# Optimization experiments

Hardware: AMD Instinct MI355X
Metric: run time of the kernel (lower is better)

Reference implementation:

```python
import jax, jax.numpy as jnp
import numpy as np

DIM = 768
NUM_HEADS = 12
HEAD_DIM = DIM // NUM_HEADS
SCALE = HEAD_DIM ** -0.5


def setup_inputs() -> dict:
    key = jax.random.key(0)
    ks = jax.random.split(key, 9)
    B, L, C = 4, 1024, DIM
    x = jax.random.normal(ks[0], (B, L, C), jnp.float32)
    q_ape = jax.random.normal(ks[1], (1, L, C), jnp.float32)
    k_ape = jax.random.normal(ks[2], (1, L, C), jnp.float32)
    attn_pos = jax.random.normal(ks[3], (1, NUM_HEADS, L, L), jnp.float32)
    s = C ** -0.5
    # torch Linear weights: (out_features, in_features)
    Wq = jax.random.normal(ks[4], (C, C), jnp.float32) * s
    Wk = jax.random.normal(ks[5], (C, C), jnp.float32) * s
    Wv = jax.random.normal(ks[6], (C, C), jnp.float32) * s
    Wp = jax.random.normal(ks[7], (C, C), jnp.float32) * s
    bp = jax.random.normal(ks[8], (C,), jnp.float32) * 0.01
    return {"x": x, "q_ape": q_ape, "k_ape": k_ape, "attn_pos": attn_pos,
            "Wq": Wq, "Wk": Wk, "Wv": Wv, "Wp": Wp, "bp": bp}


def _split_heads(t):
    # (B, L, C) -> (B, H, L, D)
    B, L, C = t.shape
    return t.reshape(B, L, NUM_HEADS, HEAD_DIM).transpose(0, 2, 1, 3)


def reference(x, q_ape, k_ape, attn_pos, Wq, Wk, Wv, Wp, bp):
    B, L, C = x.shape
    q = _split_heads((x + q_ape) @ Wq.T)          # (B,H,L,D)
    k = _split_heads((x + k_ape) @ Wk.T)          # (B,H,L,D)
    v = _split_heads(x @ Wv.T)                    # (B,H,L,D)
    attn = jnp.einsum('bhqd,bhkd->bhqk', q, k) * SCALE + attn_pos
    attn = jax.nn.softmax(attn, axis=-1)
    out = jnp.einsum('bhqk,bhkd->bhqd', attn, v)  # (B,H,L,D)
    out = out.transpose(0, 2, 1, 3).reshape(B, L, C)
    return out @ Wp.T + bp
```

## Files before the change

### kernel.cpp

```cpp
#include <hip/hip_runtime.h>
#include <stdint.h>

#define NH 12
#define HD 64
#define NB 4
#define SEQ 1024
#define CDIM 768
#define MTOT (NB*SEQ)
#define MC   (MTOT*CDIM)
#define LC   (SEQ*CDIM)
#define WSZ  (CDIM*CDIM)
#define LST  104
#define EST  136
#define L2E  1.44269504f

typedef __attribute__((ext_vector_type(4))) float f32x4;
typedef __attribute__((ext_vector_type(8))) __bf16 bf16x8;
typedef __attribute__((ext_vector_type(8))) short short8;
typedef __attribute__((ext_vector_type(4))) unsigned short ushort4v;
typedef unsigned short u16;

static __device__ __forceinline__ f32x4 mfma16(short8 a, short8 b, f32x4 c) {
  return __builtin_amdgcn_mfma_f32_16x16x32_bf16(
      __builtin_bit_cast(bf16x8, a), __builtin_bit_cast(bf16x8, b), c, 0, 0, 0);
}
static __device__ __forceinline__ u16 f2bf(float f) {
  unsigned u = __float_as_uint(f);
  u += 0x7FFFu + ((u >> 16) & 1u);
  return (u16)(u >> 16);
}
static __device__ __forceinline__ float bf2f(u16 h) {
  return __uint_as_float(((unsigned)h) << 16);
}
static __device__ __forceinline__ void lds_load16(const void* g, void* l) {
  __builtin_amdgcn_global_load_lds(
      (const __attribute__((address_space(1))) void*)g,
      (__attribute__((address_space(3))) void*)l, 16, 0, 0);
}
static __device__ __forceinline__ void barrier_lgkm() {
  __builtin_amdgcn_s_waitcnt(0xC07F);
  __builtin_amdgcn_s_barrier();
}

#define PREP_BLKS (MC / 4 / 256)
#define CONV_N4   ((4 * WSZ + CDIM) / 4)
#define CONV_BLKS ((CONV_N4 + 255) / 256)
__global__ __launch_bounds__(256) void prep_all(
    const float* __restrict__ xp, const float* __restrict__ qp,
    const float* __restrict__ kp, const float* __restrict__ Wq,
    const float* __restrict__ Wk, const float* __restrict__ Wv,
    const float* __restrict__ Wp, const float* __restrict__ bp,
    u16* __restrict__ Xq, u16* __restrict__ Xk, u16* __restrict__ Xv,
    u16* __restrict__ Wb) {
  int bid = blockIdx.x;
  if (bid < PREP_BLKS) {
    int i4 = bid * 256 + threadIdx.x;
    int a4 = i4 % (LC / 4);
    f32x4 xx = ((const f32x4*)xp)[i4];
    f32x4 qq = ((const f32x4*)qp)[a4];
    f32x4 kk = ((const f32x4*)kp)[a4];
    ushort4v oq, ok, ov;
#pragma unroll
    for (int j = 0; j < 4; j++) {
      oq[j] = f2bf(xx[j] + qq[j]);
      ok[j] = f2bf(xx[j] + kk[j]);
      ov[j] = f2bf(xx[j]);
    }
    ((ushort4v*)Xq)[i4] = oq;
    ((ushort4v*)Xk)[i4] = ok;
    ((ushort4v*)Xv)[i4] = ov;
  } else {
    int i4 = (bid - PREP_BLKS) * 256 + threadIdx.x;
    if (i4 >= CONV_N4) return;
    int sel = i4 / (WSZ / 4);
    int off = i4 - sel * (WSZ / 4);
    const float* src = sel == 0 ? Wq : sel == 1 ? Wk : sel == 2 ? Wv
                     : sel == 3 ? Wp : bp;
    f32x4 v = ((const f32x4*)src)[off];
    ushort4v o;
#pragma unroll
    for (int j = 0; j < 4; j++) o[j] = f2bf(v[j]);
    ((ushort4v*)Wb)[i4] = o;
  }
}

static __device__ __forceinline__ void gemm_core(
    const u16* __restrict__ Ab, const u16* __restrict__ Wb,
    short* As, short* Bs, f32x4 acc[4][4]) {
  const int t = threadIdx.x;
  const int lane = t & 63, w = t >> 6, quad = lane >> 4, l16 = lane & 15;
  const int wm = (w >> 1) * 64, wn = (w & 1) * 64;
  const int row4 = t >> 2, chunk = (t & 3) * 8;
  for (int k0 = 0; k0 < CDIM; k0 += 64) {
#pragma unroll
    for (int hh = 0; hh < 2; hh++) {
      const u16* ga = Ab + row4 * CDIM + k0 + hh * 32 + chunk;
      const u16* gb = Wb + row4 * CDIM + k0 + hh * 32 + chunk;
      lds_load16(ga,             (char*)As + hh * 8192 + t * 16);
      lds_load16(ga + 64 * CDIM, (char*)As + hh * 8192 + 4096 + t * 16);
      lds_load16(gb,             (char*)Bs + hh * 8192 + t * 16);
      lds_load16(gb + 64 * CDIM, (char*)Bs + hh * 8192 + 4096 + t * 16);
    }
    __syncthreads();
#pragma unroll
    for (int hh = 0; hh < 2; hh++) {
      const short* Ah = As + hh * 4096;
      const short* Bh = Bs + hh * 4096;
      short8 af[4], bw[4];
#pragma unroll
      for (int i = 0; i < 4; i++)
        af[i] = *(const short8*)(Ah + (wm + i * 16 + l16) * 32 + quad * 8);
#pragma unroll
      for (int j = 0; j < 4; j++)
        bw[j] = *(const short8*)(Bh + (wn + j * 16 + l16) * 32 + quad * 8);
#pragma unroll
      for (int i = 0; i < 4; i++)
#pragma unroll
        for (int j = 0; j < 4; j++)
          acc[i][j] = mfma16(af[i], bw[j], acc[i][j]);
    }
    __syncthreads();
  }
}

__global__ __launch_bounds__(256) void gemm_qkv(
    const u16* __restrict__ Xq, const u16* __restrict__ Xk, const u16* __restrict__ Xv,
    const u16* __restrict__ Wq, const u16* __restrict__ Wk, const u16* __restrict__ Wv,
    u16* __restrict__ Q, u16* __restrict__ K, u16* __restrict__ Vt) {
  __shared__ __align__(16) short S[128 * EST];
  short* As = S;
  short* Bs = S + 8192;
  const int z = blockIdx.z;
  const int m0 = blockIdx.y * 128, n0 = blockIdx.x * 128;
  const u16* A = (z == 0 ? Xq : z == 1 ? Xk : Xv) + m0 * CDIM;
  const u16* W = (z == 0 ? Wq : z == 1 ? Wk : Wv) + n0 * CDIM;
  f32x4 acc[4][4];
#pragma unroll
  for (int i = 0; i < 4; i++)
#pragma unroll
    for (int j = 0; j < 4; j++) acc[i][j] = 0.f;
  gemm_core(A, W, As, Bs, acc);

  const int t = threadIdx.x, lane = t & 63, w = t >> 6;
  const int quad = lane >> 4, l16 = lane & 15;
  const int wm = (w >> 1) * 64, wn = (w & 1) * 64;
  const float qs = (z == 0) ? 0.125f : 1.0f;

#pragma unroll
  for (int i = 0; i < 4; i++)
#pragma unroll
    for (int j = 0; j < 4; j++)
#pragma unroll
      for (int r = 0; r < 4; r++) {
        int mr = wm + i * 16 + quad * 4 + r;
        int nc = wn + j * 16 + l16;
        if (z < 2) S[mr * EST + nc] = (short)f2bf(acc[i][j][r] * qs);
        else       S[nc * EST + mr] = (short)f2bf(acc[i][j][r]);
      }
  __syncthreads();

  const int row = t >> 3, ch = t & 7;
  const int b = m0 >> 10, lbase = m0 & 1023;
  if (z < 2) {
    u16* O = (z == 0 ? Q : K);
#pragma unroll
    for (int cp = 0; cp < 2; cp++) {
      int h = (n0 >> 6) + cp;
#pragma unroll
      for (int rp = 0; rp < 4; rp++) {
        int mr = row + rp * 32;
        short8 v = *(const short8*)(S + mr * EST + cp * 64 + ch * 8);
        *(short8*)(O + ((((b * NH + h) << 10) + lbase + mr) * HD) + ch * 8) = v;
      }
    }
  } else {
#pragma unroll
    for (int rp = 0; rp < 4; rp++) {
      int rn = row + rp * 32;
      int h = (n0 + rn) >> 6, d = (n0 + rn) & 63;
#pragma unroll
      for (int cp = 0; cp < 2; cp++) {
        short8 v = *(const short8*)(S + rn * EST + cp * 64 + ch * 8);
        *(short8*)(Vt + ((b * NH + h) * HD + d) * SEQ + lbase + cp * 64 + ch * 8) = v;
      }
    }
  }
}

struct AttnCtx {
  const u16 *Kg, *Vg; const float* Pg;
  short *Ks, *Vs, *Pw;
  int sr, sc, quad, l16;
  short8 qa0, qa1;
  short8 kr0, kr1, vr0, vr1;
  f32x4 o[4];
  float lrow[4];
};

static __device__ __forceinline__ void attn_tile(
    AttnCtx& c, int kt, float (&pin)[16], float (&pout)[16], bool pre) {
  barrier_lgkm();
  *(short8*)(c.Ks + c.sr * LST + c.sc)        = c.kr0;
  *(short8*)(c.Ks + (c.sr + 32) * LST + c.sc) = c.kr1;
  *(short8*)(c.Vs + c.sr * LST + c.sc)        = c.vr0;
  *(short8*)(c.Vs + (c.sr + 32) * LST + c.sc) = c.vr1;
  if (pre) {
    const int k1 = (kt + 1) * 64;
    const u16* kg = c.Kg + k1 * HD;
    c.kr0 = *(const short8*)(kg + c.sr * HD + c.sc);
    c.kr1 = *(const short8*)(kg + (c.sr + 32) * HD + c.sc);
    const u16* vg = c.Vg + k1;
    c.vr0 = *(const short8*)(vg + c.sr * SEQ + c.sc);
    c.vr1 = *(const short8*)(vg + (c.sr + 32) * SEQ + c.sc);
    const float* pg = c.Pg + k1;
#pragma unroll
    for (int j = 0; j < 4; j++)
#pragma unroll
      for (int r = 0; r < 4; r++)
        pout[j * 4 + r] = pg[(c.quad * 4 + r) * SEQ + j * 16 + c.l16] * L2E;
  }
  barrier_lgkm();

  const int quad = c.quad, l16 = c.l16;
  f32x4 s[4];
#pragma unroll
  for (int j = 0; j < 4; j++) {
    short8 kb0 = *(const short8*)(c.Ks + (j * 16 + l16) * LST + quad * 8);
    short8 kb1 = *(const short8*)(c.Ks + (j * 16 + l16) * LST + 32 + quad * 8);
    f32x4 zz = 0.f;
    s[j] = mfma16(c.qa1, kb1, mfma16(c.qa0, kb0, zz));
  }

#pragma unroll
  for (int j = 0; j < 4; j++)
#pragma unroll
    for (int r = 0; r < 4; r++) {
      float e = __builtin_amdgcn_exp2f(fmaf(s[j][r], L2E, pin[j * 4 + r]));
      unsigned bits = __float_as_uint(e);
      c.Pw[(quad * 4 + r) * LST + j * 16 + l16] = (short)(bits >> 16);
      c.lrow[r] += __uint_as_float(bits & 0xFFFF0000u);
    }

  short8 pa0 = *(const short8*)(c.Pw + l16 * LST + quad * 8);
  short8 pa1 = *(const short8*)(c.Pw + l16 * LST + 32 + quad * 8);
#pragma unroll
  for (int j = 0; j < 4; j++) {
    short8 vb0 = *(const short8*)(c.Vs + (j * 16 + l16) * LST + quad * 8);
    short8 vb1 = *(const short8*)(c.Vs + (j * 16 + l16) * LST + 32 + quad * 8);
    c.o[j] = mfma16(pa1, vb1, mfma16(pa0, vb0, c.o[j]));
  }
}

__global__ __launch_bounds__(256) void attn(
    const u16* __restrict__ Q, const u16* __restrict__ K, const u16* __restrict__ Vt,
    const float* __restrict__ pos, u16* __restrict__ O) {
  __shared__ __align__(16) short Ks[64 * LST], Vs[64 * LST], Ps[64 * LST];
  const int t = threadIdx.x, lane = t & 63, w = t >> 6;
  const int qt = blockIdx.x, bh = blockIdx.y;
  const int b = bh / NH, h = bh % NH;
  const int q0 = qt * 64 + w * 16;

  AttnCtx c;
  c.quad = lane >> 4; c.l16 = lane & 15;
  c.sr = t >> 3; c.sc = (t & 7) * 8;
  c.Ks = Ks; c.Vs = Vs; c.Pw = Ps + w * 16 * LST;
  c.Kg = K + bh * SEQ * HD;
  c.Vg = Vt + bh * HD * SEQ;
  c.Pg = pos + (size_t)(h * SEQ + q0) * SEQ;

  const u16* Qg = Q + (bh * SEQ + q0) * HD;
  c.qa0 = *(const short8*)(Qg + c.l16 * HD + c.quad * 8);
  c.qa1 = *(const short8*)(Qg + c.l16 * HD + 32 + c.quad * 8);

#pragma unroll
  for (int j = 0; j < 4; j++) c.o[j] = 0.f;
#pragma unroll
  for (int r = 0; r < 4; r++) c.lrow[r] = 0.f;

  c.kr0 = *(const short8*)(c.Kg + c.sr * HD + c.sc);
  c.kr1 = *(const short8*)(c.Kg + (c.sr + 32) * HD + c.sc);
  c.vr0 = *(const short8*)(c.Vg + c.sr * SEQ + c.sc);
  c.vr1 = *(const short8*)(c.Vg + (c.sr + 32) * SEQ + c.sc);
  float pfA[16], pfB[16];
#pragma unroll
  for (int j = 0; j < 4; j++)
#pragma unroll
    for (int r = 0; r < 4; r++)
      pfA[j * 4 + r] = c.Pg[(c.quad * 4 + r) * SEQ + j * 16 + c.l16] * L2E;

#pragma unroll 1
  for (int kt = 0; kt < 16; kt += 2) {
    attn_tile(c, kt, pfA, pfB, true);
    attn_tile(c, kt + 1, pfB, pfA, kt + 1 < 15);
  }

#pragma unroll
  for (int off = 1; off < 16; off <<= 1)
#pragma unroll
    for (int r = 0; r < 4; r++) c.lrow[r] += __shfl_xor(c.lrow[r], off);

  u16* Og = O + (b * SEQ + q0) * CDIM + h * HD;
  float inv[4];
#pragma unroll
  for (int r = 0; r < 4; r++) inv[r] = 1.0f / c.lrow[r];
#pragma unroll
  for (int j = 0; j < 4; j++)
#pragma unroll
    for (int r = 0; r < 4; r++)
      Og[(c.quad * 4 + r) * CDIM + j * 16 + c.l16] = f2bf(c.o[j][r] * inv[r]);
}

__global__ __launch_bounds__(256) void gemm_proj(
    const u16* __restrict__ Oin, const u16* __restrict__ Wp,
    const u16* __restrict__ bp, float* __restrict__ out) {
  __shared__ __align__(16) short As[8192], Bs[8192];
  const int m0 = blockIdx.y * 128, n0 = blockIdx.x * 128;
  f32x4 acc[4][4];
#pragma unroll
  for (int i = 0; i < 4; i++)
#pragma unroll
    for (int j = 0; j < 4; j++) acc[i][j] = 0.f;
  gemm_core(Oin + m0 * CDIM, Wp + n0 * CDIM, As, Bs, acc);

  const int t = threadIdx.x, lane = t & 63, w = t >> 6;
  const int quad = lane >> 4, l16 = lane & 15;
  const int wm = (w >> 1) * 64, wn = (w & 1) * 64;
#pragma unroll
  for (int i = 0; i < 4; i++) {
    int mrow = m0 + wm + i * 16 + quad * 4;
#pragma unroll
    for (int j = 0; j < 4; j++) {
      int n = n0 + wn + j * 16 + l16;
      float bias = bf2f(bp[n]);
#pragma unroll
      for (int r = 0; r < 4; r++)
        out[(mrow + r) * CDIM + n] = acc[i][j][r] + bias;
    }
  }
}

extern "C" void kernel_launch(void* const* d_in, const int* in_sizes, int n_in,
                              void* d_out, int out_size, void* d_ws, size_t ws_size,
                              hipStream_t stream) {
  (void)in_sizes; (void)n_in; (void)out_size;
  const size_t OFF_XQ = 0, OFF_XK = (size_t)MC, OFF_XV = 2ull * MC,
               OFF_Q = 3ull * MC, OFF_K = 4ull * MC, OFF_VT = 5ull * MC,
               OFF_W = 6ull * MC, TOT = OFF_W + 4ull * WSZ + 1024;
  const size_t NEED = 2 * TOT;
  if (ws_size < NEED) return;

  u16* ws = (u16*)d_ws;
  u16 *Xq = ws + OFF_XQ, *Xk = ws + OFF_XK, *Xv = ws + OFF_XV;
  u16 *Qb = ws + OFF_Q, *Kb = ws + OFF_K, *Vt = ws + OFF_VT;
  u16 *Wb = ws + OFF_W;
  u16 *Wqb = Wb, *Wkb = Wb + WSZ, *Wvb = Wb + 2ull * WSZ,
      *Wpb = Wb + 3ull * WSZ, *bpb = Wb + 4ull * WSZ;
  u16* Ob = Xq;

  prep_all<<<PREP_BLKS + CONV_BLKS, 256, 0, stream>>>(
      (const float*)d_in[0], (const float*)d_in[1], (const float*)d_in[2],
      (const float*)d_in[4], (const float*)d_in[5], (const float*)d_in[6],
      (const float*)d_in[7], (const float*)d_in[8], Xq, Xk, Xv, Wb);
  gemm_qkv<<<dim3(6, 32, 3), 256, 0, stream>>>(Xq, Xk, Xv, Wqb, Wkb, Wvb,
                                               Qb, Kb, Vt);
  attn<<<dim3(16, 48), 256, 0, stream>>>(Qb, Kb, Vt, (const float*)d_in[3], Ob);
  gemm_proj<<<dim3(6, 32), 256, 0, stream>>>(Ob, Wpb, bpb, (float*)d_out);
}
```

Measured before the change: 217.5 us.

## Store K and V in MFMA fragment order and load directly from global

The QKV GEMM epilogue now writes K and V in a pre-swizzled layout that matches the MFMA operand fragments. The attention kernel can then load each wave's K/V operands straight from global memory into registers, with no LDS staging and no block barriers. Blocks are remapped through a 1D grid so that blocks sharing a head and its attn_pos rows are grouped, and launch bounds request 3 blocks per CU. The cost is that every wave reads K/V independently from global memory or L2 instead of sharing one LDS copy, and register pressure goes up.

Measured after the change: 218.2 us. About the same (+0.4%).

```diff
diff --git a/kernel.cpp b/kernel.cpp
--- a/kernel.cpp
+++ b/kernel.cpp
@@ -13,6 +13,7 @@
 #define LST  104
 #define EST  136
 #define L2E  1.44269504f
+#define BHSZ (SEQ*HD)
 
 typedef __attribute__((ext_vector_type(4))) float f32x4;
 typedef __attribute__((ext_vector_type(8))) __bf16 bf16x8;
@@ -36,10 +37,6 @@
   __builtin_amdgcn_global_load_lds(
       (const __attribute__((address_space(1))) void*)g,
       (__attribute__((address_space(3))) void*)l, 16, 0, 0);
-}
-static __device__ __forceinline__ void barrier_lgkm() {
-  __builtin_amdgcn_s_waitcnt(0xC07F);
-  __builtin_amdgcn_s_barrier();
 }
 
 #define PREP_BLKS (MC / 4 / 256)
@@ -161,8 +158,7 @@
 
   const int row = t >> 3, ch = t & 7;
   const int b = m0 >> 10, lbase = m0 & 1023;
-  if (z < 2) {
-    u16* O = (z == 0 ? Q : K);
+  if (z == 0) {
 #pragma unroll
     for (int cp = 0; cp < 2; cp++) {
       int h = (n0 >> 6) + cp;
@@ -170,144 +166,142 @@
       for (int rp = 0; rp < 4; rp++) {
         int mr = row + rp * 32;
         short8 v = *(const short8*)(S + mr * EST + cp * 64 + ch * 8);
-        *(short8*)(O + ((((b * NH + h) << 10) + lbase + mr) * HD) + ch * 8) = v;
+        *(short8*)(Q + ((((size_t)(b * NH + h)) << 10) + lbase + mr) * HD + ch * 8) = v;
+      }
+    }
+  } else if (z == 1) {
+#pragma unroll
+    for (int cp = 0; cp < 2; cp++) {
+      int h = (n0 >> 6) + cp;
+      u16* Kp = K + (size_t)(b * NH + h) * BHSZ;
+#pragma unroll
+      for (int rp = 0; rp < 4; rp++) {
+        int mr = row + rp * 32;
+        int tok = lbase + mr;
+        short8 v = *(const short8*)(S + mr * EST + cp * 64 + ch * 8);
+        *(short8*)(Kp + (((tok >> 4) * 8 + ch) * 16 + (tok & 15)) * 8) = v;
       }
     }
   } else {
 #pragma unroll
     for (int rp = 0; rp < 4; rp++) {
       int rn = row + rp * 32;
-      int h = (n0 + rn) >> 6, d = (n0 + rn) & 63;
+      int h = (n0 + rn) >> 6, d = rn & 63;
+      u16* Vp = Vt + (size_t)(b * NH + h) * BHSZ;
+      int jv = d >> 4, ld16 = d & 15;
 #pragma unroll
       for (int cp = 0; cp < 2; cp++) {
+        int tok = lbase + cp * 64 + ch * 8;
         short8 v = *(const short8*)(S + rn * EST + cp * 64 + ch * 8);
-        *(short8*)(Vt + ((b * NH + h) * HD + d) * SEQ + lbase + cp * 64 + ch * 8) = v;
-      }
-    }
-  }
-}
-
-struct AttnCtx {
-  const u16 *Kg, *Vg; const float* Pg;
-  short *Ks, *Vs, *Pw;
-  int sr, sc, quad, l16;
-  short8 qa0, qa1;
-  short8 kr0, kr1, vr0, vr1;
+        *(short8*)(Vp + ((((tok >> 6) * 4 + jv) * 8 + ((tok >> 3) & 7)) * 16 + ld16) * 8) = v;
+      }
+    }
+  }
+}
+
+__global__ __launch_bounds__(256, 3) void attn(
+    const u16* __restrict__ Q, const u16* __restrict__ Kf, const u16* __restrict__ Vf,
+    const float* __restrict__ pos, u16* __restrict__ O) {
+  __shared__ __align__(16) short Ps[4 * 16 * LST];
+  const int t = threadIdx.x, lane = t & 63, w = t >> 6;
+  const int quad = lane >> 4, l16 = lane & 15;
+
+  const int lid = blockIdx.x;
+  const int k8 = lid & 7, m = lid >> 3;
+  const int g = k8 * 24 + (m >> 2), b = m & 3;
+  const int h = g >> 4, qt = g & 15;
+  const int bh = b * NH + h;
+  const int q0 = qt * 64 + w * 16;
+
+  const u16* Kg = Kf + (size_t)bh * BHSZ;
+  const u16* Vg = Vf + (size_t)bh * BHSZ;
+  const float* Pg = pos + (size_t)(h * SEQ + q0) * SEQ;
+  short* Pw = Ps + w * 16 * LST;
+  const int fo = quad * 128 + l16 * 8;
+
+  const u16* Qg = Q + ((size_t)bh * SEQ + q0) * HD;
+  const short8 qa0 = *(const short8*)(Qg + l16 * HD + quad * 8);
+  const short8 qa1 = *(const short8*)(Qg + l16 * HD + 32 + quad * 8);
+
   f32x4 o[4];
   float lrow[4];
-};
-
-static __device__ __forceinline__ void attn_tile(
-    AttnCtx& c, int kt, float (&pin)[16], float (&pout)[16], bool pre) {
-  barrier_lgkm();
-  *(short8*)(c.Ks + c.sr * LST + c.sc)        = c.kr0;
-  *(short8*)(c.Ks + (c.sr + 32) * LST + c.sc) = c.kr1;
-  *(short8*)(c.Vs + c.sr * LST + c.sc)        = c.vr0;
-  *(short8*)(c.Vs + (c.sr + 32) * LST + c.sc) = c.vr1;
-  if (pre) {
-    const int k1 = (kt + 1) * 64;
-    const u16* kg = c.Kg + k1 * HD;
-    c.kr0 = *(const short8*)(kg + c.sr * HD + c.sc);
-    c.kr1 = *(const short8*)(kg + (c.sr + 32) * HD + c.sc);
-    const u16* vg = c.Vg + k1;
-    c.vr0 = *(const short8*)(vg + c.sr * SEQ + c.sc);
-    c.vr1 = *(const short8*)(vg + (c.sr + 32) * SEQ + c.sc);
-    const float* pg = c.Pg + k1;
+#pragma unroll
+  for (int j = 0; j < 4; j++) o[j] = 0.f;
+#pragma unroll
+  for (int r = 0; r < 4; r++) lrow[r] = 0.f;
+
+  short8 kb0[4], kb1[4];
+  float pf[16];
+#pragma unroll
+  for (int j = 0; j < 4; j++) {
+    kb0[j] = *(const short8*)(Kg + j * 1024 + fo);
+    kb1[j] = *(const short8*)(Kg + j * 1024 + 512 + fo);
+  }
+#pragma unroll
+  for (int j = 0; j < 4; j++)
+#pragma unroll
+    for (int r = 0; r < 4; r++)
+      pf[j * 4 + r] = Pg[(quad * 4 + r) * SEQ + j * 16 + l16] * L2E;
+
+#pragma unroll 1
+  for (int kt = 0; kt < 16; ++kt) {
+    const int kbase = kt * 4096;
+    short8 vb0[4], vb1[4];
+#pragma unroll
+    for (int j = 0; j < 4; j++) {
+      vb0[j] = *(const short8*)(Vg + kbase + j * 1024 + fo);
+      vb1[j] = *(const short8*)(Vg + kbase + j * 1024 + 512 + fo);
+    }
+    f32x4 s[4];
+#pragma unroll
+    for (int j = 0; j < 4; j++) {
+      f32x4 zz = 0.f;
+      s[j] = mfma16(qa1, kb1[j], mfma16(qa0, kb0[j], zz));
+    }
 #pragma unroll
     for (int j = 0; j < 4; j++)
 #pragma unroll
-      for (int r = 0; r < 4; r++)
-        pout[j * 4 + r] = pg[(c.quad * 4 + r) * SEQ + j * 16 + c.l16] * L2E;
-  }
-  barrier_lgkm();
-
-  const int quad = c.quad, l16 = c.l16;
-  f32x4 s[4];
-#pragma unroll
-  for (int j = 0; j < 4; j++) {
-    short8 kb0 = *(const short8*)(c.Ks + (j * 16 + l16) * LST + quad * 8);
-    short8 kb1 = *(const short8*)(c.Ks + (j * 16 + l16) * LST + 32 + quad * 8);
-    f32x4 zz = 0.f;
-    s[j] = mfma16(c.qa1, kb1, mfma16(c.qa0, kb0, zz));
-  }
-
+      for (int r = 0; r < 4; r++) {
+        float e = __builtin_amdgcn_exp2f(fmaf(s[j][r], L2E, pf[j * 4 + r]));
+        unsigned bits = __float_as_uint(e);
+        Pw[(quad * 4 + r) * LST + j * 16 + l16] = (short)(bits >> 16);
+        lrow[r] += __uint_as_float(bits & 0xFFFF0000u);
+      }
+    if (kt < 15) {
+      const int nb = kbase + 4096;
+#pragma unroll
+      for (int j = 0; j < 4; j++) {
+        kb0[j] = *(const short8*)(Kg + nb + j * 1024 + fo);
+        kb1[j] = *(const short8*)(Kg + nb + j * 1024 + 512 + fo);
+      }
+      const float* pg = Pg + (kt + 1) * 64;
+#pragma unroll
+      for (int j = 0; j < 4; j++)
+#pragma unroll
+        for (int r = 0; r < 4; r++)
+          pf[j * 4 + r] = pg[(quad * 4 + r) * SEQ + j * 16 + l16] * L2E;
+    }
+    const short8 pa0 = *(const short8*)(Pw + l16 * LST + quad * 8);
+    const short8 pa1 = *(const short8*)(Pw + l16 * LST + 32 + quad * 8);
+#pragma unroll
+    for (int j = 0; j < 4; j++)
+      o[j] = mfma16(pa1, vb1[j], mfma16(pa0, vb0[j], o[j]));
+  }
+
+#pragma unroll
+  for (int off = 1; off < 16; off <<= 1)
+#pragma unroll
+    for (int r = 0; r < 4; r++) lrow[r] += __shfl_xor(lrow[r], off);
+
+  u16* Og = O + ((size_t)b * SEQ + q0) * CDIM + h * HD;
+  float inv[4];
+#pragma unroll
+  for (int r = 0; r < 4; r++) inv[r] = 1.0f / lrow[r];
 #pragma unroll
   for (int j = 0; j < 4; j++)
 #pragma unroll
-    for (int r = 0; r < 4; r++) {
-      float e = __builtin_amdgcn_exp2f(fmaf(s[j][r], L2E, pin[j * 4 + r]));
-      unsigned bits = __float_as_uint(e);
-      c.Pw[(quad * 4 + r) * LST + j * 16 + l16] = (short)(bits >> 16);
-      c.lrow[r] += __uint_as_float(bits & 0xFFFF0000u);
-    }
-
-  short8 pa0 = *(const short8*)(c.Pw + l16 * LST + quad * 8);
-  short8 pa1 = *(const short8*)(c.Pw + l16 * LST + 32 + quad * 8);
-#pragma unroll
-  for (int j = 0; j < 4; j++) {
-    short8 vb0 = *(const short8*)(c.Vs + (j * 16 + l16) * LST + quad * 8);
-    short8 vb1 = *(const short8*)(c.Vs + (j * 16 + l16) * LST + 32 + quad * 8);
-    c.o[j] = mfma16(pa1, vb1, mfma16(pa0, vb0, c.o[j]));
-  }
-}
-
-__global__ __launch_bounds__(256) void attn(
-    const u16* __restrict__ Q, const u16* __restrict__ K, const u16* __restrict__ Vt,
-    const float* __restrict__ pos, u16* __restrict__ O) {
-  __shared__ __align__(16) short Ks[64 * LST], Vs[64 * LST], Ps[64 * LST];
-  const int t = threadIdx.x, lane = t & 63, w = t >> 6;
-  const int qt = blockIdx.x, bh = blockIdx.y;
-  const int b = bh / NH, h = bh % NH;
-  const int q0 = qt * 64 + w * 16;
-
-  AttnCtx c;
-  c.quad = lane >> 4; c.l16 = lane & 15;
-  c.sr = t >> 3; c.sc = (t & 7) * 8;
-  c.Ks = Ks; c.Vs = Vs; c.Pw = Ps + w * 16 * LST;
-  c.Kg = K + bh * SEQ * HD;
-  c.Vg = Vt + bh * HD * SEQ;
-  c.Pg = pos + (size_t)(h * SEQ + q0) * SEQ;
-
-  const u16* Qg = Q + (bh * SEQ + q0) * HD;
-  c.qa0 = *(const short8*)(Qg + c.l16 * HD + c.quad * 8);
-  c.qa1 = *(const short8*)(Qg + c.l16 * HD + 32 + c.quad * 8);
-
-#pragma unroll
-  for (int j = 0; j < 4; j++) c.o[j] = 0.f;
-#pragma unroll
-  for (int r = 0; r < 4; r++) c.lrow[r] = 0.f;
-
-  c.kr0 = *(const short8*)(c.Kg + c.sr * HD + c.sc);
-  c.kr1 = *(const short8*)(c.Kg + (c.sr + 32) * HD + c.sc);
-  c.vr0 = *(const short8*)(c.Vg + c.sr * SEQ + c.sc);
-  c.vr1 = *(const short8*)(c.Vg + (c.sr + 32) * SEQ + c.sc);
-  float pfA[16], pfB[16];
-#pragma unroll
-  for (int j = 0; j < 4; j++)
-#pragma unroll
     for (int r = 0; r < 4; r++)
-      pfA[j * 4 + r] = c.Pg[(c.quad * 4 + r) * SEQ + j * 16 + c.l16] * L2E;
-
-#pragma unroll 1
-  for (int kt = 0; kt < 16; kt += 2) {
-    attn_tile(c, kt, pfA, pfB, true);
-    attn_tile(c, kt + 1, pfB, pfA, kt + 1 < 15);
-  }
-
-#pragma unroll
-  for (int off = 1; off < 16; off <<= 1)
-#pragma unroll
-    for (int r = 0; r < 4; r++) c.lrow[r] += __shfl_xor(c.lrow[r], off);
-
-  u16* Og = O + (b * SEQ + q0) * CDIM + h * HD;
-  float inv[4];
-#pragma unroll
-  for (int r = 0; r < 4; r++) inv[r] = 1.0f / c.lrow[r];
-#pragma unroll
-  for (int j = 0; j < 4; j++)
-#pragma unroll
-    for (int r = 0; r < 4; r++)
-      Og[(c.quad * 4 + r) * CDIM + j * 16 + c.l16] = f2bf(c.o[j][r] * inv[r]);
+      Og[(quad * 4 + r) * CDIM + j * 16 + l16] = f2bf(o[j][r] * inv[r]);
 }
 
 __global__ __launch_bounds__(256) void gemm_proj(
@@ -363,6 +357,6 @@
       (const float*)d_in[7], (const float*)d_in[8], Xq, Xk, Xv, Wb);
   gemm_qkv<<<dim3(6, 32, 3), 256, 0, stream>>>(Xq, Xk, Xv, Wqb, Wkb, Wvb,
                                                Qb, Kb, Vt);
-  attn<<<dim3(16, 48), 256, 0, stream>>>(Qb, Kb, Vt, (const float*)d_in[3], Ob);
+  attn<<<dim3(768), 256, 0, stream>>>(Qb, Kb, Vt, (const float*)d_in[3], Ob);
   gemm_proj<<<dim3(6, 32), 256, 0, stream>>>(Ob, Wpb, bpb, (float*)d_out);
 }
```
